# Kernel tuning notes

Measured on AMD Instinct MI355X. Metric: run time of the kernel, lower is better.

The kernel has to match this reference:

```python
import jax, jax.numpy as jnp
import numpy as np

N_NODES = 50000
N_EDGES = 800000
IN_DIM = 64
HIDDEN = 64
N_LAYERS = 3
IMPROVED_FILL = 2.0  # improved_gcn=True -> self-loop weight 2
BN_EPS = 1e-5


def setup_inputs() -> dict:
    key = jax.random.key(0)
    ks = jax.random.split(key, 8)
    node_features = jax.random.normal(ks[0], (N_NODES, IN_DIM), dtype=jnp.float32)
    edge_indices = jax.random.randint(ks[1], (2, N_EDGES), 0, N_NODES, dtype=jnp.int64)
    edge_weight = jax.random.uniform(ks[2], (N_EDGES,), dtype=jnp.float32)
    # stacked per-layer params (in_dim == hidden_dim so weights stack cleanly)
    glorot = 1.0 / np.sqrt(HIDDEN)
    Ws = jax.random.uniform(ks[3], (N_LAYERS, HIDDEN, HIDDEN), minval=-glorot, maxval=glorot, dtype=jnp.float32)
    bs = jnp.zeros((N_LAYERS, HIDDEN), dtype=jnp.float32)
    gammas = jnp.ones((N_LAYERS, HIDDEN), dtype=jnp.float32)
    betas = jnp.zeros((N_LAYERS, HIDDEN), dtype=jnp.float32)
    return {"node_features": node_features, "edge_indices": edge_indices,
            "edge_weight": edge_weight, "Ws": Ws, "bs": bs,
            "gammas": gammas, "betas": betas}


def _gcn_layer(x, src, dst, w, W, b, gamma, beta):
    # GCNConv: x' = D^-1/2 (A + 2I) D^-1/2 (x W) + b  (improved=True)
    n = x.shape[0]
    lin = x @ W  # [N, H]
    loop_idx = jnp.arange(n, dtype=src.dtype)
    s = jnp.concatenate([src, loop_idx])
    d = jnp.concatenate([dst, loop_idx])
    wf = jnp.concatenate([w, jnp.full((n,), IMPROVED_FILL, dtype=w.dtype)])
    deg = jax.ops.segment_sum(wf, d, num_segments=n)
    dinv = jnp.where(deg > 0, jax.lax.rsqrt(deg), 0.0)
    norm = dinv[s] * wf * dinv[d]  # [E+N]
    agg = jax.ops.segment_sum(lin[s] * norm[:, None], d, num_segments=n)  # scatter-add
    h = jax.nn.relu(agg + b)
    # BatchNorm1d (training-mode batch stats, biased variance)
    mu = jnp.mean(h, axis=0)
    var = jnp.mean(jnp.square(h - mu), axis=0)
    h = (h - mu) * jax.lax.rsqrt(var + BN_EPS) * gamma + beta
    # Dropout treated as identity (eval / deterministic reference)
    return h


def reference(node_features, edge_indices, edge_weight, Ws, bs, gammas, betas):
    src, dst = edge_indices[0], edge_indices[1]
    h = node_features
    reps = []
    for i in range(N_LAYERS):
        h = _gcn_layer(h, src, dst, edge_weight, Ws[i], bs[i], gammas[i], betas[i])
        reps.append(h)
    return jnp.stack(reps)  # [n_layers, N, H] stacked intermediate reps
```

## Files before the change

kernel.cpp:

```cpp
#include <hip/hip_runtime.h>
#include <hip/hip_bf16.h>
#include <hip/hip_fp16.h>

#define N_NODES 50000
#define N_EDGES 800000
#define HID 64
#define N_LAYERS 3
#define BN_EPS 1e-5f
#define SELF_W 2.0f
#define BUCKET 48
#define NXCD 8
#define DSTRANGE 6250
#define GPB 1563
#define GN 196
#define GS 9375
#define GG 1563
#define GL 3125
#define GA 12500
#define NSTATS 128
#define Q18 262144.0f
#define Q18INV (1.0f / 262144.0f)

__device__ __forceinline__ unsigned short f2bf(float f) {
    return (unsigned short)((__float_as_uint(f) + 0x8000u) >> 16);
}
__device__ __forceinline__ float bf2f(unsigned short u) {
    return __uint_as_float(((unsigned)u) << 16);
}


__global__ void k_init(unsigned* __restrict__ packed4, float* __restrict__ statsP) {
    int i = blockIdx.x * blockDim.x + threadIdx.x;
    if (i < N_NODES) packed4[i] = 0u;
    if (i < NSTATS * 128) statsP[i] = 0.f;
}

__global__ void k_place(const int* __restrict__ src, const int* __restrict__ dst,
                        const float* __restrict__ w, unsigned* __restrict__ packed4,
                        unsigned* __restrict__ entries) {
    int group = blockIdx.x & (NXCD - 1);
    int big = blockIdx.x >> 3;
    int lo = group * DSTRANGE, hi = lo + DSTRANGE;
    int base = big * 512 + threadIdx.x;
#pragma unroll
    for (int r = 0; r < 2; ++r) {
        int e = base + r * 256;
        if (e < N_EDGES) {
            int d = dst[e];
            if (d >= lo && d < hi) {
                float wv = w[e];
                unsigned q = (unsigned)(wv * Q18 + 0.5f);
                unsigned old = atomicAdd(&packed4[d], (1u << 24) | q);
                int slot = (int)(old >> 24);
                unsigned hb = (unsigned)__half_as_ushort(__float2half(wv));
                entries[d * BUCKET + slot] = (hb << 16) | (unsigned)src[e];
            }
        }
    }
}

__global__ void k_norm_lin0(const unsigned* __restrict__ packed4,
                            unsigned* __restrict__ entries, float* __restrict__ selfnorm,
                            const float* __restrict__ x, const float* __restrict__ W0,
                            unsigned short* __restrict__ lin) {
    int tid = threadIdx.x;
    if (blockIdx.x < GS) {
        int idx = blockIdx.x * 256 + tid;
        int node = idx / BUCKET;
        int slot = idx - node * BUCKET;
        if (node < N_NODES) {
            unsigned pn = packed4[node];
            float din = rsqrtf(SELF_W + (float)(pn & 0xFFFFFFu) * Q18INV);
            if (slot == 0) selfnorm[node] = SELF_W * din * din;
            int cnt = (int)(pn >> 24);
            if (slot < cnt) {
                unsigned u = entries[idx];
                unsigned s = u & 0xFFFFu;
                float wv = __half2float(__ushort_as_half((unsigned short)(u >> 16)));
                unsigned ps = packed4[s];
                float dis = rsqrtf(SELF_W + (float)(ps & 0xFFFFFFu) * Q18INV);
                float n = wv * din * dis;
                entries[idx] = ((__float_as_uint(n) + 0x8000u) & 0xFFFF0000u) | s;
            }
        }
        return;
    }
    __shared__ float sW[HID * HID];
    __shared__ float sh[16][HID];
    for (int k = tid; k < HID * HID; k += 256) sW[k] = W0[k];
    int r = tid >> 6, c = tid & 63;
    int row0 = (blockIdx.x - GS) * 16;
#pragma unroll
    for (int i = 0; i < 4; ++i) {
        int row = row0 + r * 4 + i;
        sh[r * 4 + i][c] = x[(size_t)row * HID + c];
    }
    __syncthreads();
    float a0 = 0.f, a1 = 0.f, a2 = 0.f, a3 = 0.f;
#pragma unroll
    for (int k = 0; k < HID; ++k) {
        float wv = sW[k * HID + c];
        a0 = fmaf(sh[r * 4 + 0][k], wv, a0);
        a1 = fmaf(sh[r * 4 + 1][k], wv, a1);
        a2 = fmaf(sh[r * 4 + 2][k], wv, a2);
        a3 = fmaf(sh[r * 4 + 3][k], wv, a3);
    }
    lin[(size_t)(row0 + r * 4 + 0) * HID + c] = f2bf(a0);
    lin[(size_t)(row0 + r * 4 + 1) * HID + c] = f2bf(a1);
    lin[(size_t)(row0 + r * 4 + 2) * HID + c] = f2bf(a2);
    lin[(size_t)(row0 + r * 4 + 3) * HID + c] = f2bf(a3);
}


__global__ void k_gather(const unsigned short* __restrict__ lin,
                         const unsigned* __restrict__ entries,
                         const unsigned* __restrict__ packed4,
                         const float* __restrict__ selfnorm,
                         const float* __restrict__ b, float* __restrict__ out,
                         float* __restrict__ statsP) {
    int tid = threadIdx.x;
    int wslot = __builtin_amdgcn_readfirstlane(tid >> 6);
    int nbase = blockIdx.x * 32 + wslot * 4;
    int lane = tid & 63;
    int g = lane >> 4;
    int quad = lane & 15;
    const ushort4* lin4 = (const ushort4*)lin;
    int n0 = nbase, n1 = nbase + 1, n2 = nbase + 2, n3 = nbase + 3;
    int c0 = (n0 < N_NODES) ? (int)(packed4[n0] >> 24) : 0;
    int c1 = (n1 < N_NODES) ? (int)(packed4[n1] >> 24) : 0;
    int c2 = (n2 < N_NODES) ? (int)(packed4[n2] >> 24) : 0;
    int c3 = (n3 < N_NODES) ? (int)(packed4[n3] >> 24) : 0;
    const unsigned* ep0 = entries + (size_t)(n0 < N_NODES ? n0 : 0) * BUCKET;
    const unsigned* ep1 = entries + (size_t)(n1 < N_NODES ? n1 : 0) * BUCKET;
    const unsigned* ep2 = entries + (size_t)(n2 < N_NODES ? n2 : 0) * BUCKET;
    const unsigned* ep3 = entries + (size_t)(n3 < N_NODES ? n3 : 0) * BUCKET;
    float a00 = 0.f, a01 = 0.f, a02 = 0.f, a03 = 0.f;
    float a10 = 0.f, a11 = 0.f, a12 = 0.f, a13 = 0.f;
    float a20 = 0.f, a21 = 0.f, a22 = 0.f, a23 = 0.f;
    float a30 = 0.f, a31 = 0.f, a32 = 0.f, a33 = 0.f;
    int cm01 = c0 > c1 ? c0 : c1;
    int cm23 = c2 > c3 ? c2 : c3;
    int cmax = cm01 > cm23 ? cm01 : cm23;
    for (int k = 0; k < cmax; k += 16) {
        unsigned e0[16], e1[16], e2[16], e3[16];
#pragma unroll
        for (int j = 0; j < 16; ++j) {
            e0[j] = ep0[k + j]; e1[j] = ep1[k + j];
            e2[j] = ep2[k + j]; e3[j] = ep3[k + j];
        }
#pragma unroll
        for (int j = 0; j < 4; ++j) {
            unsigned s0 = (g == 0) ? e0[j*4] : ((g == 1) ? e0[j*4+1] : ((g == 2) ? e0[j*4+2] : e0[j*4+3]));
            unsigned s1 = (g == 0) ? e1[j*4] : ((g == 1) ? e1[j*4+1] : ((g == 2) ? e1[j*4+2] : e1[j*4+3]));
            unsigned s2 = (g == 0) ? e2[j*4] : ((g == 1) ? e2[j*4+1] : ((g == 2) ? e2[j*4+2] : e2[j*4+3]));
            unsigned s3 = (g == 0) ? e3[j*4] : ((g == 1) ? e3[j*4+1] : ((g == 2) ? e3[j*4+2] : e3[j*4+3]));
            int kk = k + j * 4 + g;
            s0 = (kk < c0) ? s0 : 0u;
            s1 = (kk < c1) ? s1 : 0u;
            s2 = (kk < c2) ? s2 : 0u;
            s3 = (kk < c3) ? s3 : 0u;
            ushort4 u0 = lin4[(size_t)(s0 & 0xFFFFu) * 16 + quad];
            ushort4 u1 = lin4[(size_t)(s1 & 0xFFFFu) * 16 + quad];
            ushort4 u2 = lin4[(size_t)(s2 & 0xFFFFu) * 16 + quad];
            ushort4 u3 = lin4[(size_t)(s3 & 0xFFFFu) * 16 + quad];
            float nn0 = __uint_as_float(s0 & 0xFFFF0000u);
            float nn1 = __uint_as_float(s1 & 0xFFFF0000u);
            float nn2 = __uint_as_float(s2 & 0xFFFF0000u);
            float nn3 = __uint_as_float(s3 & 0xFFFF0000u);
            a00 = fmaf(bf2f(u0.x), nn0, a00); a01 = fmaf(bf2f(u0.y), nn0, a01);
            a02 = fmaf(bf2f(u0.z), nn0, a02); a03 = fmaf(bf2f(u0.w), nn0, a03);
            a10 = fmaf(bf2f(u1.x), nn1, a10); a11 = fmaf(bf2f(u1.y), nn1, a11);
            a12 = fmaf(bf2f(u1.z), nn1, a12); a13 = fmaf(bf2f(u1.w), nn1, a13);
            a20 = fmaf(bf2f(u2.x), nn2, a20); a21 = fmaf(bf2f(u2.y), nn2, a21);
            a22 = fmaf(bf2f(u2.z), nn2, a22); a23 = fmaf(bf2f(u2.w), nn2, a23);
            a30 = fmaf(bf2f(u3.x), nn3, a30); a31 = fmaf(bf2f(u3.y), nn3, a31);
            a32 = fmaf(bf2f(u3.z), nn3, a32); a33 = fmaf(bf2f(u3.w), nn3, a33);
        }
    }
    a00 += __shfl_xor(a00, 16); a01 += __shfl_xor(a01, 16);
    a02 += __shfl_xor(a02, 16); a03 += __shfl_xor(a03, 16);
    a10 += __shfl_xor(a10, 16); a11 += __shfl_xor(a11, 16);
    a12 += __shfl_xor(a12, 16); a13 += __shfl_xor(a13, 16);
    a20 += __shfl_xor(a20, 16); a21 += __shfl_xor(a21, 16);
    a22 += __shfl_xor(a22, 16); a23 += __shfl_xor(a23, 16);
    a30 += __shfl_xor(a30, 16); a31 += __shfl_xor(a31, 16);
    a32 += __shfl_xor(a32, 16); a33 += __shfl_xor(a33, 16);
    a00 += __shfl_xor(a00, 32); a01 += __shfl_xor(a01, 32);
    a02 += __shfl_xor(a02, 32); a03 += __shfl_xor(a03, 32);
    a10 += __shfl_xor(a10, 32); a11 += __shfl_xor(a11, 32);
    a12 += __shfl_xor(a12, 32); a13 += __shfl_xor(a13, 32);
    a20 += __shfl_xor(a20, 32); a21 += __shfl_xor(a21, 32);
    a22 += __shfl_xor(a22, 32); a23 += __shfl_xor(a23, 32);
    a30 += __shfl_xor(a30, 32); a31 += __shfl_xor(a31, 32);
    a32 += __shfl_xor(a32, 32); a33 += __shfl_xor(a33, 32);
    __shared__ float ls[32][HID], ls2[32][HID];
    int node = (g == 0) ? n0 : ((g == 1) ? n1 : ((g == 2) ? n2 : n3));
    float b0 = (g == 0) ? a00 : ((g == 1) ? a10 : ((g == 2) ? a20 : a30));
    float b1 = (g == 0) ? a01 : ((g == 1) ? a11 : ((g == 2) ? a21 : a31));
    float b2 = (g == 0) ? a02 : ((g == 1) ? a12 : ((g == 2) ? a22 : a32));
    float b3 = (g == 0) ? a03 : ((g == 1) ? a13 : ((g == 2) ? a23 : a33));
    int rr = wslot * 4 + g;
    int cb = quad * 4;
    float4 t = make_float4(0.f, 0.f, 0.f, 0.f);
    if (node < N_NODES) {
        ushort4 u = lin4[(size_t)node * 16 + quad];
        float sn = selfnorm[node];
        float4 b4 = ((const float4*)b)[quad];
        t.x = fmaf(bf2f(u.x), sn, b0) + b4.x;
        t.y = fmaf(bf2f(u.y), sn, b1) + b4.y;
        t.z = fmaf(bf2f(u.z), sn, b2) + b4.z;
        t.w = fmaf(bf2f(u.w), sn, b3) + b4.w;
        t.x = t.x > 0.f ? t.x : 0.f;
        t.y = t.y > 0.f ? t.y : 0.f;
        t.z = t.z > 0.f ? t.z : 0.f;
        t.w = t.w > 0.f ? t.w : 0.f;
        ((float4*)out)[(size_t)node * 16 + quad] = t;
    }
    ls[rr][cb + 0] = t.x; ls[rr][cb + 1] = t.y;
    ls[rr][cb + 2] = t.z; ls[rr][cb + 3] = t.w;
    ls2[rr][cb + 0] = t.x * t.x; ls2[rr][cb + 1] = t.y * t.y;
    ls2[rr][cb + 2] = t.z * t.z; ls2[rr][cb + 3] = t.w * t.w;
    __syncthreads();
    float* sp = statsP + (size_t)(blockIdx.x & (NSTATS - 1)) * 128;
    if (tid < HID) {
        float s = 0.f;
#pragma unroll
        for (int rv = 0; rv < 32; ++rv) s += ls[rv][tid];
        atomicAdd(&sp[tid], s);
    } else if (tid < 2 * HID) {
        int cc = tid - HID;
        float s = 0.f;
#pragma unroll
        for (int rv = 0; rv < 32; ++rv) s += ls2[rv][cc];
        atomicAdd(&sp[HID + cc], s);
    }
}

__global__ void k_finalize(float* __restrict__ statsP, const float* __restrict__ gamma,
                           const float* __restrict__ beta, float* __restrict__ scsf) {
    int tid = threadIdx.x;
    if (tid < HID) {
        float s = 0.f, s2 = 0.f;
        for (int i = 0; i < NSTATS; ++i) {
            s  += statsP[i * 128 + tid];
            s2 += statsP[i * 128 + HID + tid];
        }
        const float invn = 1.0f / (float)N_NODES;
        float mu = s * invn;
        float var = s2 * invn - mu * mu;
        float sc = rsqrtf(var + BN_EPS) * gamma[tid];
        scsf[tid] = sc;
        scsf[HID + tid] = beta[tid] - mu * sc;
    }
    __syncthreads();
    for (int i = tid; i < NSTATS * 128; i += 128) statsP[i] = 0.f;
}

__global__ void k_bnlin(float* __restrict__ h, const float* __restrict__ scsf,
                        const float* __restrict__ W, unsigned short* __restrict__ lin) {
    __shared__ float sW[HID * HID];
    __shared__ float sh[16][HID];
    int tid = threadIdx.x;
    for (int k = tid; k < HID * HID; k += 256) sW[k] = W[k];
    int r = tid >> 6, c = tid & 63;
    float sc = scsf[c], sf = scsf[HID + c];
    int row0 = blockIdx.x * 16;
#pragma unroll
    for (int i = 0; i < 4; ++i) {
        int row = row0 + r * 4 + i;
        float val = h[(size_t)row * HID + c] * sc + sf;
        h[(size_t)row * HID + c] = val;
        sh[r * 4 + i][c] = val;
    }
    __syncthreads();
    float a0 = 0.f, a1 = 0.f, a2 = 0.f, a3 = 0.f;
#pragma unroll
    for (int k = 0; k < HID; ++k) {
        float wv = sW[k * HID + c];
        a0 = fmaf(sh[r * 4 + 0][k], wv, a0);
        a1 = fmaf(sh[r * 4 + 1][k], wv, a1);
        a2 = fmaf(sh[r * 4 + 2][k], wv, a2);
        a3 = fmaf(sh[r * 4 + 3][k], wv, a3);
    }
    lin[(size_t)(row0 + r * 4 + 0) * HID + c] = f2bf(a0);
    lin[(size_t)(row0 + r * 4 + 1) * HID + c] = f2bf(a1);
    lin[(size_t)(row0 + r * 4 + 2) * HID + c] = f2bf(a2);
    lin[(size_t)(row0 + r * 4 + 3) * HID + c] = f2bf(a3);
}

__global__ void k_bn_apply(float* __restrict__ h, const float* __restrict__ scsf) {
    int idx = blockIdx.x * blockDim.x + threadIdx.x;
    if (idx < N_NODES * HID) {
        int c = idx & 63;
        h[idx] = h[idx] * scsf[c] + scsf[HID + c];
    }
}


extern "C" void kernel_launch(void* const* d_in, const int* in_sizes, int n_in,
                              void* d_out, int out_size, void* d_ws, size_t ws_size,
                              hipStream_t stream) {
    const float* x      = (const float*)d_in[0];
    const int*   ei     = (const int*)d_in[1];
    const float* w      = (const float*)d_in[2];
    const float* Ws     = (const float*)d_in[3];
    const float* bs     = (const float*)d_in[4];
    const float* gammas = (const float*)d_in[5];
    const float* betas  = (const float*)d_in[6];
    float* out = (float*)d_out;

    const int* src = ei;
    const int* dst = ei + N_EDGES;

    unsigned* packed4 = (unsigned*)d_ws;
    unsigned* entries = packed4 + N_NODES;
    float*  selfnorm = (float*)(entries + (size_t)N_NODES * BUCKET);
    float*  statsP   = selfnorm + N_NODES;
    float*  scsf     = statsP + NSTATS * 128;
    unsigned short* lin = (unsigned short*)(scsf + 128);

    const int T = 256;

    k_init<<<GN, T, 0, stream>>>(packed4, statsP);
    k_place<<<NXCD * GPB, T, 0, stream>>>(src, dst, w, packed4, entries);
    k_norm_lin0<<<GS + GL, T, 0, stream>>>(packed4, entries, selfnorm, x, Ws, lin);

    for (int L = 0; L < N_LAYERS; ++L) {
        float* outL = out + (size_t)L * N_NODES * HID;
        const float* b  = bs + (size_t)L * HID;
        const float* g  = gammas + (size_t)L * HID;
        const float* bt = betas + (size_t)L * HID;

        k_gather<<<GG, 512, 0, stream>>>(lin, entries, packed4, selfnorm, b, outL, statsP);
        k_finalize<<<1, 128, 0, stream>>>(statsP, g, bt, scsf);
        if (L < N_LAYERS - 1) {
            const float* Wn = Ws + (size_t)(L + 1) * HID * HID;
            k_bnlin<<<GL, T, 0, stream>>>(outL, scsf, Wn, lin);
        } else {
            k_bn_apply<<<GA, T, 0, stream>>>(outL, scsf);
        }
    }
}
```

Measured before the change: 202.0 us.

## Fuse BN finalize into consumer kernels and use per-layer stats buffers

Removes the single-block k_finalize launch per layer. Every bnlin/bn_apply block now recomputes the BN scale and shift from the partial statistics, and the number of partial slots drops from 128 to 16 so that recomputation is cheap. Stats buffers become per-layer and are zeroed once in k_init, which removes the zeroing pass between layers. Output stores become nontemporal, and bn_apply is reshaped to 16 rows per block. The cost is more atomic contention on fewer stat slots and redundant per-block reduction work.

```diff
diff --git a/kernel.cpp b/kernel.cpp
--- a/kernel.cpp
+++ b/kernel.cpp
@@ -16,10 +16,11 @@
 #define GS 9375
 #define GG 1563
 #define GL 3125
-#define GA 12500
-#define NSTATS 128
+#define NSTATS 16
 #define Q18 262144.0f
 #define Q18INV (1.0f / 262144.0f)
+
+typedef float v4f __attribute__((ext_vector_type(4)));
 
 __device__ __forceinline__ unsigned short f2bf(float f) {
     return (unsigned short)((__float_as_uint(f) + 0x8000u) >> 16);
@@ -32,7 +33,7 @@
 __global__ void k_init(unsigned* __restrict__ packed4, float* __restrict__ statsP) {
     int i = blockIdx.x * blockDim.x + threadIdx.x;
     if (i < N_NODES) packed4[i] = 0u;
-    if (i < NSTATS * 128) statsP[i] = 0.f;
+    if (i < N_LAYERS * NSTATS * 128) statsP[i] = 0.f;
 }
 
 __global__ void k_place(const int* __restrict__ src, const int* __restrict__ dst,
@@ -201,25 +202,26 @@
     float b3 = (g == 0) ? a03 : ((g == 1) ? a13 : ((g == 2) ? a23 : a33));
     int rr = wslot * 4 + g;
     int cb = quad * 4;
-    float4 t = make_float4(0.f, 0.f, 0.f, 0.f);
+    float tx = 0.f, ty = 0.f, tz = 0.f, tw = 0.f;
     if (node < N_NODES) {
         ushort4 u = lin4[(size_t)node * 16 + quad];
         float sn = selfnorm[node];
         float4 b4 = ((const float4*)b)[quad];
-        t.x = fmaf(bf2f(u.x), sn, b0) + b4.x;
-        t.y = fmaf(bf2f(u.y), sn, b1) + b4.y;
-        t.z = fmaf(bf2f(u.z), sn, b2) + b4.z;
-        t.w = fmaf(bf2f(u.w), sn, b3) + b4.w;
-        t.x = t.x > 0.f ? t.x : 0.f;
-        t.y = t.y > 0.f ? t.y : 0.f;
-        t.z = t.z > 0.f ? t.z : 0.f;
-        t.w = t.w > 0.f ? t.w : 0.f;
-        ((float4*)out)[(size_t)node * 16 + quad] = t;
-    }
-    ls[rr][cb + 0] = t.x; ls[rr][cb + 1] = t.y;
-    ls[rr][cb + 2] = t.z; ls[rr][cb + 3] = t.w;
-    ls2[rr][cb + 0] = t.x * t.x; ls2[rr][cb + 1] = t.y * t.y;
-    ls2[rr][cb + 2] = t.z * t.z; ls2[rr][cb + 3] = t.w * t.w;
+        tx = fmaf(bf2f(u.x), sn, b0) + b4.x;
+        ty = fmaf(bf2f(u.y), sn, b1) + b4.y;
+        tz = fmaf(bf2f(u.z), sn, b2) + b4.z;
+        tw = fmaf(bf2f(u.w), sn, b3) + b4.w;
+        tx = tx > 0.f ? tx : 0.f;
+        ty = ty > 0.f ? ty : 0.f;
+        tz = tz > 0.f ? tz : 0.f;
+        tw = tw > 0.f ? tw : 0.f;
+        v4f t4 = { tx, ty, tz, tw };
+        __builtin_nontemporal_store(t4, &((v4f*)out)[(size_t)node * 16 + quad]);
+    }
+    ls[rr][cb + 0] = tx; ls[rr][cb + 1] = ty;
+    ls[rr][cb + 2] = tz; ls[rr][cb + 3] = tw;
+    ls2[rr][cb + 0] = tx * tx; ls2[rr][cb + 1] = ty * ty;
+    ls2[rr][cb + 2] = tz * tz; ls2[rr][cb + 3] = tw * tw;
     __syncthreads();
     float* sp = statsP + (size_t)(blockIdx.x & (NSTATS - 1)) * 128;
     if (tid < HID) {
@@ -236,11 +238,17 @@
     }
 }
 
-__global__ void k_finalize(float* __restrict__ statsP, const float* __restrict__ gamma,
-                           const float* __restrict__ beta, float* __restrict__ scsf) {
+__global__ void k_bnlin(float* __restrict__ h, const float* __restrict__ statsP,
+                        const float* __restrict__ gamma, const float* __restrict__ beta,
+                        const float* __restrict__ W, unsigned short* __restrict__ lin) {
+    __shared__ float sW[HID * HID];
+    __shared__ float sh[16][HID];
+    __shared__ float s_sc[HID], s_sf[HID];
     int tid = threadIdx.x;
+    for (int k = tid; k < HID * HID; k += 256) sW[k] = W[k];
     if (tid < HID) {
         float s = 0.f, s2 = 0.f;
+#pragma unroll
         for (int i = 0; i < NSTATS; ++i) {
             s  += statsP[i * 128 + tid];
             s2 += statsP[i * 128 + HID + tid];
@@ -249,27 +257,18 @@
         float mu = s * invn;
         float var = s2 * invn - mu * mu;
         float sc = rsqrtf(var + BN_EPS) * gamma[tid];
-        scsf[tid] = sc;
-        scsf[HID + tid] = beta[tid] - mu * sc;
-    }
-    __syncthreads();
-    for (int i = tid; i < NSTATS * 128; i += 128) statsP[i] = 0.f;
-}
-
-__global__ void k_bnlin(float* __restrict__ h, const float* __restrict__ scsf,
-                        const float* __restrict__ W, unsigned short* __restrict__ lin) {
-    __shared__ float sW[HID * HID];
-    __shared__ float sh[16][HID];
-    int tid = threadIdx.x;
-    for (int k = tid; k < HID * HID; k += 256) sW[k] = W[k];
+        s_sc[tid] = sc;
+        s_sf[tid] = beta[tid] - mu * sc;
+    }
+    __syncthreads();
     int r = tid >> 6, c = tid & 63;
-    float sc = scsf[c], sf = scsf[HID + c];
+    float sc = s_sc[c], sf = s_sf[c];
     int row0 = blockIdx.x * 16;
 #pragma unroll
     for (int i = 0; i < 4; ++i) {
         int row = row0 + r * 4 + i;
         float val = h[(size_t)row * HID + c] * sc + sf;
-        h[(size_t)row * HID + c] = val;
+        __builtin_nontemporal_store(val, &h[(size_t)row * HID + c]);
         sh[r * 4 + i][c] = val;
     }
     __syncthreads();
@@ -288,11 +287,33 @@
     lin[(size_t)(row0 + r * 4 + 3) * HID + c] = f2bf(a3);
 }
 
-__global__ void k_bn_apply(float* __restrict__ h, const float* __restrict__ scsf) {
-    int idx = blockIdx.x * blockDim.x + threadIdx.x;
-    if (idx < N_NODES * HID) {
-        int c = idx & 63;
-        h[idx] = h[idx] * scsf[c] + scsf[HID + c];
+__global__ void k_bn_apply(float* __restrict__ h, const float* __restrict__ statsP,
+                           const float* __restrict__ gamma, const float* __restrict__ beta) {
+    __shared__ float s_sc[HID], s_sf[HID];
+    int tid = threadIdx.x;
+    if (tid < HID) {
+        float s = 0.f, s2 = 0.f;
+#pragma unroll
+        for (int i = 0; i < NSTATS; ++i) {
+            s  += statsP[i * 128 + tid];
+            s2 += statsP[i * 128 + HID + tid];
+        }
+        const float invn = 1.0f / (float)N_NODES;
+        float mu = s * invn;
+        float var = s2 * invn - mu * mu;
+        float sc = rsqrtf(var + BN_EPS) * gamma[tid];
+        s_sc[tid] = sc;
+        s_sf[tid] = beta[tid] - mu * sc;
+    }
+    __syncthreads();
+    int r = tid >> 6, c = tid & 63;
+    float sc = s_sc[c], sf = s_sf[c];
+    int row0 = blockIdx.x * 16;
+#pragma unroll
+    for (int i = 0; i < 4; ++i) {
+        int row = row0 + r * 4 + i;
+        float val = h[(size_t)row * HID + c] * sc + sf;
+        __builtin_nontemporal_store(val, &h[(size_t)row * HID + c]);
     }
 }
 
@@ -316,8 +337,7 @@
     unsigned* entries = packed4 + N_NODES;
     float*  selfnorm = (float*)(entries + (size_t)N_NODES * BUCKET);
     float*  statsP   = selfnorm + N_NODES;
-    float*  scsf     = statsP + NSTATS * 128;
-    unsigned short* lin = (unsigned short*)(scsf + 128);
+    unsigned short* lin = (unsigned short*)(statsP + N_LAYERS * NSTATS * 128);
 
     const int T = 256;
 
@@ -330,14 +350,14 @@
         const float* b  = bs + (size_t)L * HID;
         const float* g  = gammas + (size_t)L * HID;
         const float* bt = betas + (size_t)L * HID;
-
-        k_gather<<<GG, 512, 0, stream>>>(lin, entries, packed4, selfnorm, b, outL, statsP);
-        k_finalize<<<1, 128, 0, stream>>>(statsP, g, bt, scsf);
+        float* statsL = statsP + (size_t)L * NSTATS * 128;
+
+        k_gather<<<GG, 512, 0, stream>>>(lin, entries, packed4, selfnorm, b, outL, statsL);
         if (L < N_LAYERS - 1) {
             const float* Wn = Ws + (size_t)(L + 1) * HID * HID;
-            k_bnlin<<<GL, T, 0, stream>>>(outL, scsf, Wn, lin);
+            k_bnlin<<<GL, T, 0, stream>>>(outL, statsL, g, bt, Wn, lin);
         } else {
-            k_bn_apply<<<GA, T, 0, stream>>>(outL, scsf);
-        }
-    }
-}
+            k_bn_apply<<<GL, T, 0, stream>>>(outL, statsL, g, bt);
+        }
+    }
+}
```

Result: faster. 181.3 us (-10.3%).
